# Kernel optimization log

Hardware: AMD Instinct MI355X
Metric: run time of the kernel (lower is better)

## Reference

```python
import jax, jax.numpy as jnp
import numpy as np

B, N, L = 1, 128, 256
D_MSA, D_HID, D_PAIR = 256, 32, 128
EPS = 1e-5


def setup_inputs() -> dict:
    key = jax.random.key(0)
    ks = jax.random.split(key, 8)
    msa = jax.random.normal(ks[0], (B, N, L, D_MSA), dtype=jnp.float32)
    pair = jax.random.normal(ks[1], (B, L, L, D_PAIR), dtype=jnp.float32)
    symmids = jax.random.randint(ks[2], (1,), 0, 1, dtype=jnp.int64)
    symmsub = jax.random.randint(ks[3], (1,), 0, 1, dtype=jnp.int64)
    # learned params (lecun-normal-ish scale = 1/sqrt(fan_in))
    ln_gamma = jnp.ones((D_MSA,), jnp.float32)
    ln_beta = jnp.zeros((D_MSA,), jnp.float32)
    w_left = jax.random.normal(ks[4], (D_MSA, D_HID), jnp.float32) / np.sqrt(D_MSA)
    b_left = jnp.zeros((D_HID,), jnp.float32)
    w_right = jax.random.normal(ks[5], (D_MSA, D_HID), jnp.float32) / np.sqrt(D_MSA)
    b_right = jnp.zeros((D_HID,), jnp.float32)
    w_out = jax.random.normal(ks[6], (D_HID * D_HID, D_PAIR), jnp.float32) / np.sqrt(D_HID * D_HID)
    b_out = jnp.zeros((D_PAIR,), jnp.float32)
    return {
        "msa": msa, "pair": pair, "symmids": symmids, "symmsub": symmsub,
        "ln_gamma": ln_gamma, "ln_beta": ln_beta,
        "w_left": w_left, "b_left": b_left,
        "w_right": w_right, "b_right": b_right,
        "w_out": w_out, "b_out": b_out,
    }


def reference(msa, pair, symmids, symmsub, ln_gamma, ln_beta,
              w_left, b_left, w_right, b_right, w_out, b_out):
    b, n, l, _ = msa.shape
    # LayerNorm over d_msa (biased variance, matching torch)
    mu = jnp.mean(msa, axis=-1, keepdims=True)
    var = jnp.mean(jnp.square(msa - mu), axis=-1, keepdims=True)
    x = (msa - mu) * jax.lax.rsqrt(var + EPS) * ln_gamma + ln_beta
    left = x @ w_left + b_left                       # [b, n, l, d_h]
    right = (x @ w_right + b_right) / float(n)       # [b, n, l, d_h]
    # outer product, reduced over MSA (s) dim -> [b, l, m, d_h, d_h]
    out = jnp.einsum('bsli,bsmj->blmij', left, right).reshape(b, l, l, -1)
    out = out @ w_out + b_out                        # [b, l, l, d_pair]
    return pair + out
```

## Files before the change

kernel.cpp:

```cpp
#include <hip/hip_runtime.h>


typedef float v4f __attribute__((ext_vector_type(4)));
typedef short v8s __attribute__((ext_vector_type(8)));

static __device__ inline unsigned short f2bf(float x) {
    unsigned int u = __builtin_bit_cast(unsigned int, x);
    return (unsigned short)((u + 0x7fffu + ((u >> 16) & 1u)) >> 16);
}

static __device__ inline void gl_lds16(const unsigned short* g, unsigned short* l) {
    __builtin_amdgcn_global_load_lds(
        (const __attribute__((address_space(1))) unsigned int*)g,
        (__attribute__((address_space(3))) unsigned int*)(unsigned long long)l,
        16, 0, 0);
}

__global__ __launch_bounds__(256) void k_prep(const float* __restrict__ w_out,
                                              const float* __restrict__ wl,
                                              const float* __restrict__ wr,
                                              unsigned short* __restrict__ w3,
                                              unsigned short* __restrict__ wTg) {
    const int b = blockIdx.x, t = threadIdx.x;
    unsigned short tmp[8];
    if (b < 64) {
        int tgt = b * 2048 + t * 8;
        int lane6 = (tgt >> 3) & 63, quad = lane6 >> 4, l15 = lane6 & 15;
        int w = (tgt >> 9) & 3, tt = (tgt >> 11) & 1;
        int inner = (tgt >> 12) & 1, ck = tgt >> 13;
        int p = w * 32 + tt * 16 + l15;
        for (int e = 0; e < 8; ++e) {
            int kp = ck * 64 + inner * 32 + quad * 8 + e;
            int j1 = (kp >> 9) & 1, qd = (kp >> 7) & 3, lp = (kp >> 3) & 15;
            int i1 = (kp >> 2) & 1, r = kp & 3;
            int ii = i1 * 16 + qd * 4 + r, jj = j1 * 16 + lp;
            tmp[e] = f2bf(w_out[(ii * 32 + jj) * 128 + p]);
        }
        *(uint4*)&w3[tgt] = *(const uint4*)tmp;
    } else {
        int tgt = (b - 64) * 2048 + t * 8;
        int c = tgt >> 8, d0 = tgt & 255;
        const float* src = (c < 32) ? wl : wr;
        int cc = c & 31;
        for (int e = 0; e < 8; ++e) tmp[e] = f2bf(src[(d0 + e) * 32 + cc]);
        *(uint4*)&wTg[tgt] = *(const uint4*)tmp;
    }
}

__global__ __launch_bounds__(256) void k_lnproj(
    const float* __restrict__ msa, const float* __restrict__ gamma, const float* __restrict__ beta,
    const unsigned short* __restrict__ wTg, const float* __restrict__ bl, const float* __restrict__ br,
    unsigned short* __restrict__ leftT, unsigned short* __restrict__ rightT) {
    __shared__ unsigned short xb[32 * 264];
    __shared__ unsigned short wlds[64 * 264];
    __shared__ unsigned short outT[64 * 40];

    const int t = threadIdx.x, lane = t & 63, w = t >> 6;
    const int l = blockIdx.x, s0 = blockIdx.y * 32;
    const int quad = lane >> 4, l15 = lane & 15;

    for (int it = 0; it < 8; ++it) {
        int idx = it * 2048 + t * 8;
        *(uint4*)&wlds[(idx >> 8) * 264 + (idx & 255)] = *(const uint4*)&wTg[idx];
    }

    float4 g4 = *(const float4*)&gamma[lane * 4];
    float4 be4 = *(const float4*)&beta[lane * 4];
    float4 vr[8]; float s1[8], s2[8];
    for (int r = 0; r < 8; ++r) {
        const float* row = msa + (size_t)((s0 + w * 8 + r) * 256 + l) * 256;
        vr[r] = *(const float4*)&row[lane * 4];
    }
    for (int r = 0; r < 8; ++r) {
        float4 v = vr[r];
        s1[r] = v.x + v.y + v.z + v.w;
        s2[r] = v.x * v.x + v.y * v.y + v.z * v.z + v.w * v.w;
    }
    for (int o = 32; o > 0; o >>= 1)
        for (int r = 0; r < 8; ++r) { s1[r] += __shfl_xor(s1[r], o); s2[r] += __shfl_xor(s2[r], o); }
    for (int r = 0; r < 8; ++r) {
        float mu = s1[r] * (1.f / 256);
        float rs = rsqrtf(s2[r] * (1.f / 256) - mu * mu + 1e-5f);
        float4 v = vr[r];
        ushort4 xs;
        xs.x = f2bf((v.x - mu) * rs * g4.x + be4.x);
        xs.y = f2bf((v.y - mu) * rs * g4.y + be4.y);
        xs.z = f2bf((v.z - mu) * rs * g4.z + be4.z);
        xs.w = f2bf((v.w - mu) * rs * g4.w + be4.w);
        *(ushort4*)&xb[(w * 8 + r) * 264 + lane * 4] = xs;
    }
    __syncthreads();

    const int mt = w >> 1, ntb = (w & 1) * 2;
    v4f acc[2] = {};
    const int frow = (mt * 16 + l15) * 264;
    for (int ks = 0; ks < 8; ++ks) {
        int k = ks * 32 + quad * 8;
        v8s a = *(const v8s*)&xb[frow + k];
        v8s b0 = *(const v8s*)&wlds[(ntb * 16 + l15) * 264 + k];
        v8s b1 = *(const v8s*)&wlds[((ntb + 1) * 16 + l15) * 264 + k];
        acc[0] = __builtin_amdgcn_mfma_f32_16x16x32_bf16(a, b0, acc[0], 0, 0, 0);
        acc[1] = __builtin_amdgcn_mfma_f32_16x16x32_bf16(a, b1, acc[1], 0, 0, 0);
    }

    for (int tn = 0; tn < 2; ++tn) {
        int c = (ntb + tn) * 16 + l15;
        float bias = c < 32 ? bl[c] : br[c - 32];
        float scale = c < 32 ? 1.f : (1.f / 128);
        for (int r = 0; r < 4; ++r)
            outT[c * 40 + mt * 16 + quad * 4 + r] = f2bf((acc[tn][r] + bias) * scale);
    }
    __syncthreads();

    {
        int c = t >> 2, q = t & 3;
        uint4 vv = *(const uint4*)&outT[c * 40 + q * 8];
        int cc = c & 31;
        unsigned short* base = (c < 32) ? leftT : rightT;
        unsigned short* dst = base + l * 4096 + blockIdx.y * 1024
                            + (cc >> 4) * 512 + q * 128 + (cc & 15) * 8;
        *(uint4*)dst = vv;
    }
}

__global__ __launch_bounds__(256, 4) void k_outer(
    const unsigned short* __restrict__ leftT, const unsigned short* __restrict__ rightT,
    const unsigned short* __restrict__ w2g, const float* __restrict__ bout,
    const float* __restrict__ pairIn, float* __restrict__ out) {
    __shared__ alignas(16) unsigned short smem[16384];
    unsigned short* Ah = smem;
    unsigned short* Bh = smem + 8192;
    unsigned short* Obuf = smem;

    const int t = threadIdx.x, lane = t & 63, w = t >> 6;
    const int l0 = blockIdx.x * 4, m0 = blockIdx.y * 4;
    const int wm = w & 1, wn = w >> 1;
    const int quad = lane >> 4, l15 = lane & 15;

    float pf[8];
#pragma unroll
    for (int tt = 0; tt < 2; ++tt)
#pragma unroll
        for (int r = 0; r < 4; ++r) {
            int pr = quad * 4 + r;
            int p = (w * 2 + tt) * 16 + l15;
            size_t idx = (size_t)((l0 + (pr >> 2)) * 256 + (m0 + (pr & 3))) * 128 + p;
            pf[tt * 4 + r] = pairIn[idx];
        }

    const unsigned short* Asrc = leftT + l0 * 4096;
    const unsigned short* Bsrc = rightT + m0 * 4096;

    v4f acc[4][4] = {};
    for (int kh = 0; kh < 2; ++kh) {
        if (kh) __syncthreads();
#pragma unroll
        for (int it = 0; it < 4; ++it) {
            int x = (it * 256 + t) * 8;
            gl_lds16(&Asrc[(x >> 11) * 4096 + kh * 2048 + (x & 2047)], &Ah[x]);
            gl_lds16(&Bsrc[(x >> 11) * 4096 + kh * 2048 + (x & 2047)], &Bh[x]);
        }
        __syncthreads();
#pragma unroll
        for (int kl = 0; kl < 2; ++kl) {
            v8s a[4], bb[4];
#pragma unroll
            for (int i = 0; i < 4; ++i)
                a[i] = *(const v8s*)&Ah[(wm * 2 + (i >> 1)) * 2048 + kl * 1024 + (i & 1) * 512 + lane * 8];
#pragma unroll
            for (int j = 0; j < 4; ++j)
                bb[j] = *(const v8s*)&Bh[(wn * 2 + (j >> 1)) * 2048 + kl * 1024 + (j & 1) * 512 + lane * 8];
#pragma unroll
            for (int i = 0; i < 4; ++i)
#pragma unroll
                for (int j = 0; j < 4; ++j)
                    acc[i][j] = __builtin_amdgcn_mfma_f32_16x16x32_bf16(a[i], bb[j], acc[i][j], 0, 0, 0);
        }
    }
    __syncthreads();

    const unsigned short* wsrc = w2g + w * 512 + lane * 8;
    v8s f0 = *(const v8s*)&wsrc[0];
    v8s f1 = *(const v8s*)&wsrc[2048];
    v8s f2 = *(const v8s*)&wsrc[4096];
    v8s f3 = *(const v8s*)&wsrc[6144];

    for (int a2 = 0; a2 < 2; ++a2)
        for (int b2 = 0; b2 < 2; ++b2) {
            int P = (wm * 2 + a2) * 4 + wn * 2 + b2;
            for (int j1 = 0; j1 < 2; ++j1) {
                unsigned short tmp8[8];
                for (int i1 = 0; i1 < 2; ++i1)
                    for (int r = 0; r < 4; ++r)
                        tmp8[i1 * 4 + r] = f2bf(acc[a2 * 2 + i1][b2 * 2 + j1][r]);
                int pg = (j1 * 64 + lane) ^ (P & 7) ^ ((P & 8) << 3);
                *(uint4*)&Obuf[P * 1024 + pg * 8] = *(const uint4*)tmp8;
            }
        }
    __syncthreads();

    v4f aI0[2] = {}, aI1[2] = {};
#pragma unroll
    for (int ck = 0; ck < 16; ++ck) {
        v8s c0 = f0, c1 = f1, c2 = f2, c3 = f3;
        if (ck < 15) {
            const unsigned short* nx = wsrc + (ck + 1) * 8192;
            f0 = *(const v8s*)&nx[0];
            f1 = *(const v8s*)&nx[2048];
            f2 = *(const v8s*)&nx[4096];
            f3 = *(const v8s*)&nx[6144];
        }
        {
            int g = ck * 8 + quad;
            v8s a = *(const v8s*)&Obuf[l15 * 1024 + ((g ^ (l15 & 7) ^ ((l15 & 8) << 3)) << 3)];
            aI0[0] = __builtin_amdgcn_mfma_f32_16x16x32_bf16(a, c0, aI0[0], 0, 0, 0);
            aI0[1] = __builtin_amdgcn_mfma_f32_16x16x32_bf16(a, c1, aI0[1], 0, 0, 0);
        }
        {
            int g = ck * 8 + 4 + quad;
            v8s a = *(const v8s*)&Obuf[l15 * 1024 + ((g ^ (l15 & 7) ^ ((l15 & 8) << 3)) << 3)];
            aI1[0] = __builtin_amdgcn_mfma_f32_16x16x32_bf16(a, c2, aI1[0], 0, 0, 0);
            aI1[1] = __builtin_amdgcn_mfma_f32_16x16x32_bf16(a, c3, aI1[1], 0, 0, 0);
        }
    }

#pragma unroll
    for (int tt = 0; tt < 2; ++tt) {
        int p = (w * 2 + tt) * 16 + l15;
        float bo = bout[p];
        v4f acc2 = aI0[tt] + aI1[tt];
#pragma unroll
        for (int r = 0; r < 4; ++r) {
            int pr = quad * 4 + r;
            size_t idx = (size_t)((l0 + (pr >> 2)) * 256 + (m0 + (pr & 3))) * 128 + p;
            out[idx] = pf[tt * 4 + r] + bo + acc2[r];
        }
    }
}

extern "C" void kernel_launch(void* const* d_in, const int* in_sizes, int n_in,
                              void* d_out, int out_size, void* d_ws, size_t ws_size,
                              hipStream_t stream) {
    const float* msa   = (const float*)d_in[0];
    const float* pairI = (const float*)d_in[1];
    const float* gamma = (const float*)d_in[4];
    const float* beta  = (const float*)d_in[5];
    const float* wl    = (const float*)d_in[6];
    const float* bl    = (const float*)d_in[7];
    const float* wr    = (const float*)d_in[8];
    const float* br    = (const float*)d_in[9];
    const float* wout  = (const float*)d_in[10];
    const float* bout  = (const float*)d_in[11];
    float* out = (float*)d_out;

    unsigned short* leftT  = (unsigned short*)d_ws;
    unsigned short* rightT = leftT + 256 * 32 * 128;
    unsigned short* w3     = rightT + 256 * 32 * 128;
    unsigned short* wTg    = w3 + 131072;

    k_prep<<<dim3(72), 256, 0, stream>>>(wout, wl, wr, w3, wTg);
    k_lnproj<<<dim3(256, 4), 256, 0, stream>>>(msa, gamma, beta, wTg, bl, br, leftT, rightT);
    k_outer<<<dim3(64, 64), 256, 0, stream>>>(leftT, rightT, w3, bout, pairI, out);
}
```

Baseline: 180.1 us.

## Read projection weights as pre-laid MFMA fragments and deepen w_out prefetch

```diff
diff --git a/kernel.cpp b/kernel.cpp
--- a/kernel.cpp
+++ b/kernel.cpp
@@ -20,7 +20,7 @@
                                               const float* __restrict__ wl,
                                               const float* __restrict__ wr,
                                               unsigned short* __restrict__ w3,
-                                              unsigned short* __restrict__ wTg) {
+                                              unsigned short* __restrict__ wB) {
     const int b = blockIdx.x, t = threadIdx.x;
     unsigned short tmp[8];
     if (b < 64) {
@@ -39,30 +39,30 @@
         *(uint4*)&w3[tgt] = *(const uint4*)tmp;
     } else {
         int tgt = (b - 64) * 2048 + t * 8;
-        int c = tgt >> 8, d0 = tgt & 255;
+        int frag = tgt >> 9, lane6 = (tgt >> 3) & 63;
+        int nt = frag >> 3, ks = frag & 7;
+        int quad = lane6 >> 4, l15 = lane6 & 15;
+        int c = nt * 16 + l15;
         const float* src = (c < 32) ? wl : wr;
         int cc = c & 31;
-        for (int e = 0; e < 8; ++e) tmp[e] = f2bf(src[(d0 + e) * 32 + cc]);
-        *(uint4*)&wTg[tgt] = *(const uint4*)tmp;
+        for (int e = 0; e < 8; ++e) {
+            int d = ks * 32 + quad * 8 + e;
+            tmp[e] = f2bf(src[d * 32 + cc]);
+        }
+        *(uint4*)&wB[tgt] = *(const uint4*)tmp;
     }
 }
 
 __global__ __launch_bounds__(256) void k_lnproj(
     const float* __restrict__ msa, const float* __restrict__ gamma, const float* __restrict__ beta,
-    const unsigned short* __restrict__ wTg, const float* __restrict__ bl, const float* __restrict__ br,
+    const unsigned short* __restrict__ wB, const float* __restrict__ bl, const float* __restrict__ br,
     unsigned short* __restrict__ leftT, unsigned short* __restrict__ rightT) {
     __shared__ unsigned short xb[32 * 264];
-    __shared__ unsigned short wlds[64 * 264];
     __shared__ unsigned short outT[64 * 40];
 
     const int t = threadIdx.x, lane = t & 63, w = t >> 6;
     const int l = blockIdx.x, s0 = blockIdx.y * 32;
     const int quad = lane >> 4, l15 = lane & 15;
-
-    for (int it = 0; it < 8; ++it) {
-        int idx = it * 2048 + t * 8;
-        *(uint4*)&wlds[(idx >> 8) * 264 + (idx & 255)] = *(const uint4*)&wTg[idx];
-    }
 
     float4 g4 = *(const float4*)&gamma[lane * 4];
     float4 be4 = *(const float4*)&beta[lane * 4];
@@ -94,11 +94,12 @@
     const int mt = w >> 1, ntb = (w & 1) * 2;
     v4f acc[2] = {};
     const int frow = (mt * 16 + l15) * 264;
+    const unsigned short* wBp = wB + lane * 8;
+#pragma unroll
     for (int ks = 0; ks < 8; ++ks) {
-        int k = ks * 32 + quad * 8;
-        v8s a = *(const v8s*)&xb[frow + k];
-        v8s b0 = *(const v8s*)&wlds[(ntb * 16 + l15) * 264 + k];
-        v8s b1 = *(const v8s*)&wlds[((ntb + 1) * 16 + l15) * 264 + k];
+        v8s a = *(const v8s*)&xb[frow + ks * 32 + quad * 8];
+        v8s b0 = *(const v8s*)&wBp[(ntb * 8 + ks) * 512];
+        v8s b1 = *(const v8s*)&wBp[((ntb + 1) * 8 + ks) * 512];
         acc[0] = __builtin_amdgcn_mfma_f32_16x16x32_bf16(a, b0, acc[0], 0, 0, 0);
         acc[1] = __builtin_amdgcn_mfma_f32_16x16x32_bf16(a, b1, acc[1], 0, 0, 0);
     }
@@ -123,7 +124,7 @@
     }
 }
 
-__global__ __launch_bounds__(256, 4) void k_outer(
+__global__ __launch_bounds__(256, 3) void k_outer(
     const unsigned short* __restrict__ leftT, const unsigned short* __restrict__ rightT,
     const unsigned short* __restrict__ w2g, const float* __restrict__ bout,
     const float* __restrict__ pairIn, float* __restrict__ out) {
@@ -180,10 +181,14 @@
     __syncthreads();
 
     const unsigned short* wsrc = w2g + w * 512 + lane * 8;
-    v8s f0 = *(const v8s*)&wsrc[0];
-    v8s f1 = *(const v8s*)&wsrc[2048];
-    v8s f2 = *(const v8s*)&wsrc[4096];
-    v8s f3 = *(const v8s*)&wsrc[6144];
+    v8s A0 = *(const v8s*)&wsrc[0];
+    v8s A1 = *(const v8s*)&wsrc[2048];
+    v8s A2 = *(const v8s*)&wsrc[4096];
+    v8s A3 = *(const v8s*)&wsrc[6144];
+    v8s B0 = *(const v8s*)&wsrc[8192];
+    v8s B1 = *(const v8s*)&wsrc[8192 + 2048];
+    v8s B2 = *(const v8s*)&wsrc[8192 + 4096];
+    v8s B3 = *(const v8s*)&wsrc[8192 + 6144];
 
     for (int a2 = 0; a2 < 2; ++a2)
         for (int b2 = 0; b2 < 2; ++b2) {
@@ -201,26 +206,40 @@
 
     v4f aI0[2] = {}, aI1[2] = {};
 #pragma unroll
-    for (int ck = 0; ck < 16; ++ck) {
-        v8s c0 = f0, c1 = f1, c2 = f2, c3 = f3;
-        if (ck < 15) {
-            const unsigned short* nx = wsrc + (ck + 1) * 8192;
-            f0 = *(const v8s*)&nx[0];
-            f1 = *(const v8s*)&nx[2048];
-            f2 = *(const v8s*)&nx[4096];
-            f3 = *(const v8s*)&nx[6144];
-        }
+    for (int ck = 0; ck < 16; ck += 2) {
         {
             int g = ck * 8 + quad;
             v8s a = *(const v8s*)&Obuf[l15 * 1024 + ((g ^ (l15 & 7) ^ ((l15 & 8) << 3)) << 3)];
-            aI0[0] = __builtin_amdgcn_mfma_f32_16x16x32_bf16(a, c0, aI0[0], 0, 0, 0);
-            aI0[1] = __builtin_amdgcn_mfma_f32_16x16x32_bf16(a, c1, aI0[1], 0, 0, 0);
+            aI0[0] = __builtin_amdgcn_mfma_f32_16x16x32_bf16(a, A0, aI0[0], 0, 0, 0);
+            aI0[1] = __builtin_amdgcn_mfma_f32_16x16x32_bf16(a, A1, aI0[1], 0, 0, 0);
+            int g2 = ck * 8 + 4 + quad;
+            v8s a2 = *(const v8s*)&Obuf[l15 * 1024 + ((g2 ^ (l15 & 7) ^ ((l15 & 8) << 3)) << 3)];
+            aI1[0] = __builtin_amdgcn_mfma_f32_16x16x32_bf16(a2, A2, aI1[0], 0, 0, 0);
+            aI1[1] = __builtin_amdgcn_mfma_f32_16x16x32_bf16(a2, A3, aI1[1], 0, 0, 0);
+            if (ck + 2 < 16) {
+                const unsigned short* nx = wsrc + (ck + 2) * 8192;
+                A0 = *(const v8s*)&nx[0];
+                A1 = *(const v8s*)&nx[2048];
+                A2 = *(const v8s*)&nx[4096];
+                A3 = *(const v8s*)&nx[6144];
+            }
         }
         {
-            int g = ck * 8 + 4 + quad;
+            int g = (ck + 1) * 8 + quad;
             v8s a = *(const v8s*)&Obuf[l15 * 1024 + ((g ^ (l15 & 7) ^ ((l15 & 8) << 3)) << 3)];
-            aI1[0] = __builtin_amdgcn_mfma_f32_16x16x32_bf16(a, c2, aI1[0], 0, 0, 0);
-            aI1[1] = __builtin_amdgcn_mfma_f32_16x16x32_bf16(a, c3, aI1[1], 0, 0, 0);
+            aI0[0] = __builtin_amdgcn_mfma_f32_16x16x32_bf16(a, B0, aI0[0], 0, 0, 0);
+            aI0[1] = __builtin_amdgcn_mfma_f32_16x16x32_bf16(a, B1, aI0[1], 0, 0, 0);
+            int g2 = (ck + 1) * 8 + 4 + quad;
+            v8s a2 = *(const v8s*)&Obuf[l15 * 1024 + ((g2 ^ (l15 & 7) ^ ((l15 & 8) << 3)) << 3)];
+            aI1[0] = __builtin_amdgcn_mfma_f32_16x16x32_bf16(a2, B2, aI1[0], 0, 0, 0);
+            aI1[1] = __builtin_amdgcn_mfma_f32_16x16x32_bf16(a2, B3, aI1[1], 0, 0, 0);
+            if (ck + 3 < 16) {
+                const unsigned short* nx = wsrc + (ck + 3) * 8192;
+                B0 = *(const v8s*)&nx[0];
+                B1 = *(const v8s*)&nx[2048];
+                B2 = *(const v8s*)&nx[4096];
+                B3 = *(const v8s*)&nx[6144];
+            }
         }
     }
 
@@ -256,9 +275,9 @@
     unsigned short* leftT  = (unsigned short*)d_ws;
     unsigned short* rightT = leftT + 256 * 32 * 128;
     unsigned short* w3     = rightT + 256 * 32 * 128;
-    unsigned short* wTg    = w3 + 131072;
-
-    k_prep<<<dim3(72), 256, 0, stream>>>(wout, wl, wr, w3, wTg);
-    k_lnproj<<<dim3(256, 4), 256, 0, stream>>>(msa, gamma, beta, wTg, bl, br, leftT, rightT);
+    unsigned short* wB     = w3 + 131072;
+
+    k_prep<<<dim3(72), 256, 0, stream>>>(wout, wl, wr, w3, wB);
+    k_lnproj<<<dim3(256, 4), 256, 0, stream>>>(msa, gamma, beta, wB, bl, br, leftT, rightT);
     k_outer<<<dim3(64, 64), 256, 0, stream>>>(leftT, rightT, w3, bout, pairI, out);
 }
```

Result: faster. 172.2 us (-4.4%).
